# Performance work log

Measured on AMD Instinct MI355X. Metric: run time of the kernel, lower is better.

## Reference

```python
import jax, jax.numpy as jnp
import numpy as np

D, K, B, IMG, NCH = 128, 512, 8, 128, 3


def adder2d(x, w, k, stride, pad):
    # AdderNet L1 'convolution': y[b,co,l] = -sum_p |patch[b,p,l] - w[co,p]|
    # x: [B,C,H,W], w: [Cout, C*k*k]
    p = jax.lax.conv_general_dilated_patches(x, (k, k), (stride, stride), [(pad, pad), (pad, pad)])
    Bb, P, Ho, Wo = p.shape
    p = p.reshape(Bb, P, Ho * Wo)  # [B, C*k*k, L]
    def one(wc):  # wc: [P] -> [B, L]; sequential over Cout to bound memory
        return -jnp.sum(jnp.abs(p - wc[None, :, None]), axis=1)
    o = jax.lax.map(one, w)  # [Cout, B, L]
    return jnp.transpose(o, (1, 0, 2)).reshape(Bb, w.shape[0], Ho, Wo)


def bn(x, g, b, eps=1e-5):
    # eval-mode BatchNorm2d with running_mean=0, running_var=1
    s = g * jax.lax.rsqrt(jnp.asarray(1.0 + eps, x.dtype))
    return x * s[None, :, None, None] + b[None, :, None, None]


def conv2d(x, w, b, pad):
    y = jax.lax.conv_general_dilated(x, w, (1, 1), [(pad, pad), (pad, pad)],
                                     dimension_numbers=('NCHW', 'OIHW', 'NCHW'))
    return y + b[None, :, None, None]


def up2x(x):  # nn.Upsample(scale_factor=2, bilinear, align_corners=False)
    Bb, C, H, W = x.shape
    return jax.image.resize(x, (Bb, C, 2 * H, 2 * W), method='bilinear')


def adder_resblock(x, w1, w2, g, b):
    # [ReLU, adder3x3, BN, ReLU, adder1x1] + residual
    h = jax.nn.relu(x)
    h = adder2d(h, w1, 3, 1, 1)
    h = bn(h, g, b)
    h = jax.nn.relu(h)
    h = adder2d(h, w2, 1, 1, 0)
    return x + h


def conv_resblock(x, w1, b1, w2, b2):
    # [ReLU, conv3x3, ReLU, conv1x1] + residual (bn=False in decoder)
    h = jax.nn.relu(x)
    h = conv2d(h, w1, b1, 1)
    h = jax.nn.relu(h)
    h = conv2d(h, w2, b2, 0)
    return x + h


def vq_forward(z_e, E):
    # NearestEmbed: E is [d, k]
    Bb, C, H, W = z_e.shape
    flat = jnp.transpose(z_e, (0, 2, 3, 1)).reshape(-1, C)  # [N, d]
    d2 = (jnp.sum(flat * flat, axis=1, keepdims=True)
          - 2.0 * (flat @ E) + jnp.sum(E * E, axis=0)[None, :])  # [N, k]
    argmin = jnp.argmin(d2, axis=1)  # [N]
    q = jnp.take(E.T, argmin, axis=0)  # [N, d]
    # weight_sg=True path: straight-through to z_e, no grad to E
    zq_flat = flat + jax.lax.stop_gradient(q - flat)
    z_q = jnp.transpose(zq_flat.reshape(Bb, H, W, C), (0, 3, 1, 2))
    # emb path: z_e detached, grad flows to E through the gather
    emb = jnp.transpose(q.reshape(Bb, H, W, C), (0, 3, 1, 2))
    return z_q, emb, argmin.reshape(Bb, H, W)


def reference(x, we1, we2, ae1_w1, ae1_w2, ae2_w1, ae2_w2, bn_gamma, bn_beta,
              emb_weight, rd1_w1, rd1_b1, rd1_w2, rd1_b2, rd2_w1, rd2_b1,
              rd2_w2, rd2_b2, cd1_w, cd1_b, cd2_w, cd2_b):
    g, b = bn_gamma, bn_beta
    h = adder2d(x, we1, 4, 2, 1)
    h = jax.nn.relu(bn(h, g[0], b[0]))
    h = adder2d(h, we2, 4, 2, 1)
    h = jax.nn.relu(bn(h, g[1], b[1]))
    h = adder_resblock(h, ae1_w1, ae1_w2, g[2], b[2])
    h = bn(h, g[3], b[3])
    h = adder_resblock(h, ae2_w1, ae2_w2, g[4], b[4])
    z_e = bn(h, g[5], b[5])  # bne4 (gamma = 1/40)

    z_q, emb, argmin = vq_forward(z_e, emb_weight)

    y = conv_resblock(z_q, rd1_w1, rd1_b1, rd1_w2, rd1_b2)
    y = bn(y, g[6], b[6])
    y = conv_resblock(y, rd2_w1, rd2_b1, rd2_w2, rd2_b2)
    y = up2x(y)
    y = conv2d(y, cd1_w, cd1_b, 1)
    y = jax.nn.relu(bn(y, g[7], b[7]))
    y = up2x(y)
    y = conv2d(y, cd2_w, cd2_b, 1)
    y = jnp.tanh(y)
    return (y, z_e, emb, argmin)


def setup_inputs() -> dict:
    key = jax.random.key(0)
    ks = jax.random.split(key, 16)
    f = lambda k, shp: (0.02 * jax.random.normal(k, shp)).astype(jnp.float32)
    inp = {}
    inp['x'] = jax.random.normal(ks[0], (B, NCH, IMG, IMG), jnp.float32)
    inp['we1'] = f(ks[1], (D, NCH * 16))       # adder 4x4 s2
    inp['we2'] = f(ks[2], (D, D * 16))
    inp['ae1_w1'] = f(ks[3], (D, D * 9))       # adder 3x3
    inp['ae1_w2'] = f(ks[4], (D, D))           # adder 1x1
    inp['ae2_w1'] = f(ks[5], (D, D * 9))
    inp['ae2_w2'] = f(ks[6], (D, D))
    inp['bn_gamma'] = jnp.ones((8, D), jnp.float32).at[5].set(1.0 / 40.0)
    inp['bn_beta'] = jnp.zeros((8, D), jnp.float32)
    inp['emb_weight'] = f(ks[7], (D, K))
    inp['rd1_w1'] = f(ks[8], (D, D, 3, 3)); inp['rd1_b1'] = jnp.zeros(D, jnp.float32)
    inp['rd1_w2'] = f(ks[9], (D, D, 1, 1)); inp['rd1_b2'] = jnp.zeros(D, jnp.float32)
    inp['rd2_w1'] = f(ks[10], (D, D, 3, 3)); inp['rd2_b1'] = jnp.zeros(D, jnp.float32)
    inp['rd2_w2'] = f(ks[11], (D, D, 1, 1)); inp['rd2_b2'] = jnp.zeros(D, jnp.float32)
    inp['cd1_w'] = f(ks[12], (D, D, 3, 3)); inp['cd1_b'] = jnp.zeros(D, jnp.float32)
    inp['cd2_w'] = f(ks[13], (NCH, D, 3, 3)); inp['cd2_b'] = jnp.zeros(NCH, jnp.float32)
    return inp
```

## Files before the change

### kernel.cpp

```cpp
#include <hip/hip_runtime.h>
#include <math.h>

constexpr int Dc = 128;
constexpr int Kc = 512;
constexpr int Bc = 8;

template<int ISADD, int K, int STRIDE, int PAD, int IT, int EPI, int CIN, int CH,
         int OUT_ROWS, int WOUT, int WIN, int HIN, int HOUT, int COBW, int NW,
         int KSPLIT>
__global__ __launch_bounds__(NW * 64)
void lds_layer(const float* __restrict__ x, const float* __restrict__ w,
               const float* __restrict__ bias,
               const float* __restrict__ itG, const float* __restrict__ itB,
               const float* __restrict__ res,
               const float* __restrict__ rG, const float* __restrict__ rB,
               const float* __restrict__ oG, const float* __restrict__ oB,
               float* __restrict__ out) {
  constexpr int BT = NW * 64;
  constexpr int NWG = NW / KSPLIT;
  constexpr int CINW = CIN / KSPLIT;
  constexpr int CHS = KSPLIT * CH;
  constexpr int PW = 2;
  constexpr int KK = K * K;
  constexpr int SPAN = (PW - 1) * STRIDE + K;
  constexpr int IN_ROWS = (OUT_ROWS - 1) * STRIDE + K;
  constexpr int WPAD = (WOUT - 1) * STRIDE + K;
  constexpr int WLDS = (WPAD + 3) & ~3;
  constexpr int PGW = WOUT / PW;
  static_assert(OUT_ROWS * PGW == 64, "one wave covers the pixel tile");
  static_assert(NW % KSPLIT == 0 && CIN % KSPLIT == 0 && CINW % CH == 0, "split");
  static_assert(KSPLIT == 1 ||
                NWG * 64 * PW * COBW <= CHS * IN_ROWS * WLDS, "scratch fits");
  constexpr int NBAND = HOUT / OUT_ROWS;
  constexpr int W4 = WIN / 4;
  constexpr int NELEM4 = CHS * IN_ROWS * W4;
  constexpr int NIT4 = (NELEM4 + BT - 1) / BT;
  constexpr bool EXACT = (NELEM4 % BT) == 0;
  const float r15 = rsqrtf(1.0f + 1e-5f);

  __shared__ alignas(16) float lds[CHS][IN_ROWS][WLDS];

  int tid = threadIdx.x;
  int gb = blockIdx.x;
  int cg = gb / (Bc * NBAND);
  int rem = gb % (Bc * NBAND);
  int band = rem % NBAND;
  int b = rem / NBAND;
  int wv = __builtin_amdgcn_readfirstlane(tid >> 6);
  int lane = tid & 63;
  int grp = wv / NWG;
  int wloc = wv % NWG;
  int co0 = cg * (NWG * COBW) + wloc * COBW;
  int pr = lane / PGW, pc = lane % PGW;
  int oh = band * OUT_ROWS + pr;
  int ow0 = pc * PW;
  int yi0 = band * OUT_ROWS * STRIDE - PAD;

  for (int e = tid; e < CHS * IN_ROWS * WLDS; e += BT) ((float*)lds)[e] = 0.f;

  float acc[PW][COBW];
#pragma unroll
  for (int p = 0; p < PW; ++p)
#pragma unroll
    for (int j = 0; j < COBW; ++j)
      acc[p][j] = (ISADD || grp != 0) ? 0.f : bias[co0 + j];

  const float* xb = x + (long)b * CIN * HIN * WIN;
  float4 rbuf[NIT4];

  auto stage = [&](int cc) {
#pragma unroll
    for (int it = 0; it < NIT4; ++it) {
      int e = it * BT + tid;
      if (!EXACT && e >= NELEM4) break;
      int c4 = e % W4;
      int r = (e / W4) % IN_ROWS;
      int ch2 = e / (W4 * IN_ROWS);
      int gc = cc + (ch2 % CH) + (ch2 / CH) * CINW;
      int yi = yi0 + r;
      float4 v = make_float4(0.f, 0.f, 0.f, 0.f);
      if (yi >= 0 && yi < HIN) {
        v = *(const float4*)&xb[((long)gc * HIN + yi) * WIN + 4 * c4];
        if (IT == 1) {
          v.x = fmaxf(v.x, 0.f); v.y = fmaxf(v.y, 0.f);
          v.z = fmaxf(v.z, 0.f); v.w = fmaxf(v.w, 0.f);
        }
        if (IT == 2) {
          float sc = itG[gc] * r15, bc = itB[gc];
          v.x = fmaxf(fmaf(v.x, sc, bc), 0.f);
          v.y = fmaxf(fmaf(v.y, sc, bc), 0.f);
          v.z = fmaxf(fmaf(v.z, sc, bc), 0.f);
          v.w = fmaxf(fmaf(v.w, sc, bc), 0.f);
        }
      }
      rbuf[it] = v;
    }
  };
  auto towrite = [&]() {
#pragma unroll
    for (int it = 0; it < NIT4; ++it) {
      int e = it * BT + tid;
      if (!EXACT && e >= NELEM4) break;
      int c4 = e % W4;
      int r = (e / W4) % IN_ROWS;
      int ch2 = e / (W4 * IN_ROWS);
      float* p = &lds[ch2][r][4 * c4 + PAD];
      float4 v = rbuf[it];
      p[0] = v.x; p[1] = v.y; p[2] = v.z; p[3] = v.w;
    }
  };

  stage(0);
  for (int cc = 0; cc < CINW; cc += CH) {
    __syncthreads();
    towrite();
    __syncthreads();
    if (cc + CH < CINW) stage(cc + CH);
    for (int chl = 0; chl < CH; ++chl) {
      float vbuf[K][SPAN];
#pragma unroll
      for (int kh = 0; kh < K; ++kh) {
        const float* rp0 = &lds[grp * CH + chl][pr * STRIDE + kh][ow0 * STRIDE];
        if constexpr (SPAN == 6 && (PW * STRIDE) % 4 == 0) {
          float4 a = *(const float4*)rp0;
          float2 c2 = *(const float2*)(rp0 + 4);
          vbuf[kh][0] = a.x; vbuf[kh][1] = a.y; vbuf[kh][2] = a.z;
          vbuf[kh][3] = a.w; vbuf[kh][4] = c2.x; vbuf[kh][5] = c2.y;
        } else if constexpr (SPAN == 4 && (PW * STRIDE) % 2 == 0) {
          float2 a = *(const float2*)rp0;
          float2 c2 = *(const float2*)(rp0 + 2);
          vbuf[kh][0] = a.x; vbuf[kh][1] = a.y;
          vbuf[kh][2] = c2.x; vbuf[kh][3] = c2.y;
        } else if constexpr (SPAN == 2 && (PW * STRIDE) % 2 == 0) {
          float2 a = *(const float2*)rp0;
          vbuf[kh][0] = a.x; vbuf[kh][1] = a.y;
        } else {
#pragma unroll
          for (int s = 0; s < SPAN; ++s) vbuf[kh][s] = rp0[s];
        }
      }
      const float* wc = w + ((long)co0 * CIN + (grp * CINW + cc + chl)) * KK;
#pragma unroll
      for (int kh = 0; kh < K; ++kh)
#pragma unroll
        for (int kw = 0; kw < K; ++kw)
#pragma unroll
          for (int j = 0; j < COBW; ++j) {
            float ww = wc[(long)j * CIN * KK + kh * K + kw];
#pragma unroll
            for (int p = 0; p < PW; ++p) {
              float v = vbuf[kh][p * STRIDE + kw];
              if (ISADD) acc[p][j] += fabsf(v - ww);
              else       acc[p][j] = fmaf(v, ww, acc[p][j]);
            }
          }
    }
  }

  if constexpr (KSPLIT >= 2) {
    float* scr = (float*)lds;
    int sb = (wloc * 64 + lane) * (PW * COBW);
#pragma unroll
    for (int g = 1; g < KSPLIT; ++g) {
      __syncthreads();
      if (grp == g) {
#pragma unroll
        for (int p = 0; p < PW; ++p)
#pragma unroll
          for (int j = 0; j < COBW; ++j) scr[sb + p * COBW + j] = acc[p][j];
      }
      __syncthreads();
      if (grp == 0) {
#pragma unroll
        for (int p = 0; p < PW; ++p)
#pragma unroll
          for (int j = 0; j < COBW; ++j) acc[p][j] += scr[sb + p * COBW + j];
      }
    }
    if (grp != 0) return;
  }

  long obase = ((long)(b * Dc + co0) * HOUT + oh) * WOUT + ow0;
  float* ob = out + obase;
  const float* rp = (EPI == 2 || EPI == 3 || EPI == 6) ? res + obase : nullptr;
  constexpr long hw = (long)HOUT * WOUT;
#pragma unroll
  for (int j = 0; j < COBW; ++j) {
    float og = 0.f, obb = 0.f, rg = 0.f, rbb = 0.f;
    if (EPI == 1 || EPI == 6) { og = oG[co0 + j] * r15; obb = oB[co0 + j]; }
    if (EPI == 3 || EPI == 6) { rg = rG[co0 + j] * r15; rbb = rB[co0 + j]; }
#pragma unroll
    for (int p = 0; p < PW; ++p) {
      float val = ISADD ? -acc[p][j] : acc[p][j];
      if (EPI == 1) val = fmaxf(fmaf(val, og, obb), 0.f);
      if (EPI == 2) val = rp[j * hw + p] + val;
      if (EPI == 3) val = fmaf(rp[j * hw + p], rg, rbb) + val;
      if (EPI == 5) val = fmaxf(val, 0.f);
      if (EPI == 6) val = fmaf(fmaf(rp[j * hw + p], rg, rbb) + val, og, obb);
      ob[j * hw + p] = val;
    }
  }
}

__device__ __forceinline__ void up_coef(int p, int H, int& i0, int& i1, float& w0, float& w1) {
  int m = p >> 1;
  if ((p & 1) == 0) { i0 = (m > 0) ? m - 1 : 0; i1 = m; w0 = 0.25f; w1 = 0.75f; }
  else              { i0 = m; i1 = (m + 1 < H) ? m + 1 : H - 1; w0 = 0.75f; w1 = 0.25f; }
}

__global__ void up2x_kernel(const float* __restrict__ in, float* __restrict__ out,
                            int C, int H, int W) {
  int H2 = 2 * H, W2 = 2 * W;
  int i = blockIdx.x * blockDim.x + threadIdx.x;
  int total = Bc * C * H2 * W2;
  if (i >= total) return;
  int ow = i % W2; int t = i / W2;
  int oh = t % H2; t /= H2;
  int c = t % C; int b = t / C;
  int y0, y1, x0, x1; float wy0, wy1, wx0, wx1;
  up_coef(oh, H, y0, y1, wy0, wy1);
  up_coef(ow, W, x0, x1, wx0, wx1);
  const float* p = in + (b * C + c) * H * W;
  float v = wy0 * (wx0 * p[y0 * W + x0] + wx1 * p[y0 * W + x1])
          + wy1 * (wx0 * p[y1 * W + x0] + wx1 * p[y1 * W + x1]);
  out[i] = v;
}

__global__ __launch_bounds__(256)
void conv3x3_up_tanh_quad(const float* __restrict__ x, const float* __restrict__ w,
                          const float* __restrict__ bias, float* __restrict__ out,
                          int Hs, int Ws, int Cout) {
  constexpr int CIN = Dc;
  int H2 = 2 * Hs, W2 = 2 * Ws;
  int nq = Hs * Ws;
  int i = blockIdx.x * blockDim.x + threadIdx.x;
  int total = Bc * Cout * nq;
  if (i >= total) return;
  int q = i % nq; int t = i / nq;
  int co = t % Cout; int b = t / Cout;
  int n = q % Ws, m = q / Ws;
  int rows[3] = { (m > 0) ? m - 1 : 0, m, (m + 1 < Hs) ? m + 1 : Hs - 1 };
  int cols[3] = { (n > 0) ? n - 1 : 0, n, (n + 1 < Ws) ? n + 1 : Ws - 1 };
  float rv[4] = { (2 * m - 1 >= 0) ? 1.f : 0.f, 1.f, 1.f, (2 * m + 2 < H2) ? 1.f : 0.f };
  float cv[4] = { (2 * n - 1 >= 0) ? 1.f : 0.f, 1.f, 1.f, (2 * n + 2 < W2) ? 1.f : 0.f };
  float bco = bias[co];
  float acc[4] = { bco, bco, bco, bco };
  const float* xb = x + b * CIN * nq;
  const float* wb = w + co * CIN * 9;
  for (int c = 0; c < CIN; ++c) {
    const float* xc = xb + c * nq;
    float s[3][3];
#pragma unroll
    for (int a = 0; a < 3; ++a)
#pragma unroll
      for (int e = 0; e < 3; ++e) s[a][e] = xc[rows[a] * Ws + cols[e]];
    float rb[4][3];
#pragma unroll
    for (int e = 0; e < 3; ++e) {
      rb[0][e] = fmaf(0.75f, s[0][e], 0.25f * s[1][e]);
      rb[1][e] = fmaf(0.25f, s[0][e], 0.75f * s[1][e]);
      rb[2][e] = fmaf(0.75f, s[1][e], 0.25f * s[2][e]);
      rb[3][e] = fmaf(0.25f, s[1][e], 0.75f * s[2][e]);
    }
    float u[4][4];
#pragma unroll
    for (int di = 0; di < 4; ++di) {
      float rm = rv[di];
      u[di][0] = fmaf(0.75f, rb[di][0], 0.25f * rb[di][1]) * rm * cv[0];
      u[di][1] = fmaf(0.25f, rb[di][0], 0.75f * rb[di][1]) * rm * cv[1];
      u[di][2] = fmaf(0.75f, rb[di][1], 0.25f * rb[di][2]) * rm * cv[2];
      u[di][3] = fmaf(0.25f, rb[di][1], 0.75f * rb[di][2]) * rm * cv[3];
    }
    const float* wc = wb + c * 9;
#pragma unroll
    for (int kh = 0; kh < 3; ++kh)
#pragma unroll
      for (int kw = 0; kw < 3; ++kw) {
        float ww = wc[kh * 3 + kw];
        acc[0] = fmaf(u[kh][kw],         ww, acc[0]);
        acc[1] = fmaf(u[kh][kw + 1],     ww, acc[1]);
        acc[2] = fmaf(u[kh + 1][kw],     ww, acc[2]);
        acc[3] = fmaf(u[kh + 1][kw + 1], ww, acc[3]);
      }
  }
  float* ob = out + (b * Cout + co) * H2 * W2 + (2 * m) * W2 + 2 * n;
  ob[0] = tanhf(acc[0]);      ob[1] = tanhf(acc[1]);
  ob[W2] = tanhf(acc[2]);     ob[W2 + 1] = tanhf(acc[3]);
}

__global__ void vq_e2_kernel(const float* __restrict__ E, float* __restrict__ e2) {
  int k = blockIdx.x * blockDim.x + threadIdx.x;
  if (k >= Kc) return;
  float s = 0.f;
  for (int d = 0; d < Dc; ++d) { float v = E[d * Kc + k]; s += v * v; }
  e2[k] = s;
}

__global__ __launch_bounds__(256)
void vq_kernel8(const float* __restrict__ z_e, const float* __restrict__ E,
                const float* __restrict__ e2,
                float* __restrict__ emb, float* __restrict__ argmin_out) {
  constexpr int HW = 1024;
  __shared__ float f[8][Dc];
  __shared__ float d2s[8][256];
  __shared__ int   ks[8][256];
  int tid = threadIdx.x;
  int n0 = blockIdx.x * 8;
  int b = n0 >> 10;
  int rem = n0 & 1023;
  const float* zb = z_e + (long)b * Dc * HW + rem;
#pragma unroll
  for (int i = 0; i < 4; ++i) {
    int e = i * 256 + tid;
    int p = e & 7, d = e >> 3;
    f[p][d] = zb[d * HW + p];
  }
  __syncthreads();
  float f2 = 0.f;
  if (tid < 8) {
    for (int d = 0; d < Dc; ++d) f2 += f[tid][d] * f[tid][d];
    d2s[tid][0] = f2;
  }
  __syncthreads();
  float f2v[8];
#pragma unroll
  for (int p = 0; p < 8; ++p) f2v[p] = d2s[p][0];
  __syncthreads();

  float best[8]; int bk[8];
#pragma unroll
  for (int p = 0; p < 8; ++p) { best[p] = 3.4e38f; bk[p] = 0; }
  for (int kk = tid; kk < Kc; kk += 256) {
    float dot[8];
#pragma unroll
    for (int p = 0; p < 8; ++p) dot[p] = 0.f;
    for (int d = 0; d < Dc; ++d) {
      float ed = E[d * Kc + kk];
#pragma unroll
      for (int p = 0; p < 8; ++p) dot[p] = fmaf(f[p][d], ed, dot[p]);
    }
    float e2k = e2[kk];
#pragma unroll
    for (int p = 0; p < 8; ++p) {
      float d2 = f2v[p] - 2.f * dot[p] + e2k;
      if (d2 < best[p] || (d2 == best[p] && kk < bk[p])) { best[p] = d2; bk[p] = kk; }
    }
  }
#pragma unroll
  for (int p = 0; p < 8; ++p) { d2s[p][tid] = best[p]; ks[p][tid] = bk[p]; }
  __syncthreads();
  for (int s = 128; s > 0; s >>= 1) {
    if (tid < s) {
#pragma unroll
      for (int p = 0; p < 8; ++p) {
        float ob = d2s[p][tid + s]; int ok = ks[p][tid + s];
        if (ob < d2s[p][tid] || (ob == d2s[p][tid] && ok < ks[p][tid])) {
          d2s[p][tid] = ob; ks[p][tid] = ok;
        }
      }
    }
    __syncthreads();
  }
  if (tid < 8) argmin_out[n0 + tid] = (float)ks[tid][0];
  float* eb = emb + (long)b * Dc * HW + rem;
#pragma unroll
  for (int i = 0; i < 4; ++i) {
    int e = i * 256 + tid;
    int p = e & 7, d = e >> 3;
    eb[d * HW + p] = E[d * Kc + ks[p][0]];
  }
}

extern "C" void kernel_launch(void* const* d_in, const int* in_sizes, int n_in,
                              void* d_out, int out_size, void* d_ws, size_t ws_size,
                              hipStream_t stream) {
  const float* x      = (const float*)d_in[0];
  const float* we1    = (const float*)d_in[1];
  const float* we2    = (const float*)d_in[2];
  const float* ae1_w1 = (const float*)d_in[3];
  const float* ae1_w2 = (const float*)d_in[4];
  const float* ae2_w1 = (const float*)d_in[5];
  const float* ae2_w2 = (const float*)d_in[6];
  const float* bn_g   = (const float*)d_in[7];
  const float* bn_b   = (const float*)d_in[8];
  const float* embw   = (const float*)d_in[9];
  const float* rd1_w1 = (const float*)d_in[10];
  const float* rd1_b1 = (const float*)d_in[11];
  const float* rd1_w2 = (const float*)d_in[12];
  const float* rd1_b2 = (const float*)d_in[13];
  const float* rd2_w1 = (const float*)d_in[14];
  const float* rd2_b1 = (const float*)d_in[15];
  const float* rd2_w2 = (const float*)d_in[16];
  const float* rd2_b2 = (const float*)d_in[17];
  const float* cd1_w  = (const float*)d_in[18];
  const float* cd1_b  = (const float*)d_in[19];
  const float* cd2_w  = (const float*)d_in[20];
  const float* cd2_b  = (const float*)d_in[21];

  const float* g0 = bn_g + 0 * Dc; const float* b0 = bn_b + 0 * Dc;
  const float* g1 = bn_g + 1 * Dc; const float* b1 = bn_b + 1 * Dc;
  const float* g2 = bn_g + 2 * Dc; const float* b2 = bn_b + 2 * Dc;
  const float* g3 = bn_g + 3 * Dc; const float* b3 = bn_b + 3 * Dc;
  const float* g4 = bn_g + 4 * Dc; const float* b4 = bn_b + 4 * Dc;
  const float* g5 = bn_g + 5 * Dc; const float* b5 = bn_b + 5 * Dc;
  const float* g6 = bn_g + 6 * Dc; const float* b6 = bn_b + 6 * Dc;
  const float* g7 = bn_g + 7 * Dc; const float* b7 = bn_b + 7 * Dc;

  float* W64a = (float*)d_ws;
  float* W64b = W64a + 4194304;
  float* Wa   = W64b + 4194304;
  float* Wb   = Wa + 1048576;
  float* Wc   = Wb + 1048576;
  float* e2b  = W64b;

  float* out_y   = (float*)d_out;
  float* out_ze  = out_y  + 393216;
  float* out_emb = out_ze + 1048576;
  float* out_am  = out_emb + 1048576;

  const int TB = 256;
  const int TB8 = 512;
  auto nb = [](int n) { return (n + 255) / 256; };
  const int N64 = Bc * Dc * 64 * 64;
  const float* nul = nullptr;

  const int G32s = 16 * Bc * 8;
  const int G11s = 8 * Bc * 8;
  const int Gwe1 = 8 * Bc * 32;
  const int Gcd1 = 4 * Bc * 32;

  lds_layer<1,4,2,1, 0,1, 3,3, 2,64,128,128,64, 4,4,1><<<Gwe1, TB, 0, stream>>>(
      x, we1, nul, nul, nul, nul, nul, nul, g0, b0, W64a);
  lds_layer<1,4,2,1, 0,1, Dc,2, 4,32,64,64,32, 4,8,4><<<G32s, TB8, 0, stream>>>(
      W64a, we2, nul, nul, nul, nul, nul, nul, g1, b1, Wa);
  lds_layer<1,3,1,1, 0,1, Dc,8, 4,32,32,32,32, 4,8,4><<<G32s, TB8, 0, stream>>>(
      Wa, ae1_w1, nul, nul, nul, nul, nul, nul, g2, b2, Wb);
  lds_layer<1,1,1,0, 0,2, Dc,16, 4,32,32,32,32, 8,8,4><<<G11s, TB8, 0, stream>>>(
      Wb, ae1_w2, nul, nul, nul, Wa, nul, nul, nul, nul, Wc);
  lds_layer<1,3,1,1, 2,1, Dc,8, 4,32,32,32,32, 4,8,4><<<G32s, TB8, 0, stream>>>(
      Wc, ae2_w1, nul, g3, b3, nul, nul, nul, g4, b4, Wb);
  lds_layer<1,1,1,0, 0,6, Dc,16, 4,32,32,32,32, 8,8,4><<<G11s, TB8, 0, stream>>>(
      Wb, ae2_w2, nul, nul, nul, Wc, g3, b3, g5, b5, out_ze);

  vq_e2_kernel<<<2, 256, 0, stream>>>(embw, e2b);
  vq_kernel8<<<Bc * 1024 / 8, 256, 0, stream>>>(out_ze, embw, e2b, out_emb, out_am);

  lds_layer<0,3,1,1, 1,5, Dc,8, 4,32,32,32,32, 4,8,4><<<G32s, TB8, 0, stream>>>(
      out_emb, rd1_w1, rd1_b1, nul, nul, nul, nul, nul, nul, nul, Wb);
  lds_layer<0,1,1,0, 0,2, Dc,16, 4,32,32,32,32, 8,8,4><<<G11s, TB8, 0, stream>>>(
      Wb, rd1_w2, rd1_b2, nul, nul, out_emb, nul, nul, nul, nul, Wa);
  lds_layer<0,3,1,1, 2,5, Dc,8, 4,32,32,32,32, 4,8,4><<<G32s, TB8, 0, stream>>>(
      Wa, rd2_w1, rd2_b1, g6, b6, nul, nul, nul, nul, nul, Wb);
  lds_layer<0,1,1,0, 0,3, Dc,16, 4,32,32,32,32, 8,8,4><<<G11s, TB8, 0, stream>>>(
      Wb, rd2_w2, rd2_b2, nul, nul, Wa, g6, b6, nul, nul, Wc);

  up2x_kernel<<<nb(N64), TB, 0, stream>>>(Wc, W64a, Dc, 32, 32);
  lds_layer<0,3,1,1, 0,1, Dc,8, 2,64,64,64,64, 8,8,2><<<Gcd1, TB8, 0, stream>>>(
      W64a, cd1_w, cd1_b, nul, nul, nul, nul, nul, g7, b7, W64b);

  conv3x3_up_tanh_quad<<<nb(Bc * 3 * 64 * 64), TB, 0, stream>>>(W64b, cd2_w, cd2_b, out_y, 64, 64, 3);
}
```

Measured before the change: 852.3 us.

## Add dedicated 1x1 pointwise kernel and retune LDS layer split factors

Adds a pw1x1 kernel for the four 1x1 adder/conv layers. It reads input pixels directly from global memory as float2, splits the channel reduction across 4 waves, and combines partial sums through shared memory before applying the fused epilogue. The 3x3 and 4x4 lds_layer launches are retuned to larger channel chunks, fewer output channels per workgroup and a smaller K-split. The goal is to cut LDS staging overhead for pointwise layers and improve occupancy and parallelism for the spatial layers, at the cost of weights being read from global or cache per thread.

```diff
diff --git a/kernel.cpp b/kernel.cpp
--- a/kernel.cpp
+++ b/kernel.cpp
@@ -202,6 +202,91 @@
   }
 }
 
+template<int ISADD, int EPI, int COBW>
+__global__ __launch_bounds__(256)
+void pw1x1(const float* __restrict__ x, const float* __restrict__ w,
+           const float* __restrict__ bias,
+           const float* __restrict__ res,
+           const float* __restrict__ rG, const float* __restrict__ rB,
+           const float* __restrict__ oG, const float* __restrict__ oB,
+           float* __restrict__ out) {
+  constexpr int HW = 1024;
+  constexpr int CIN = Dc;
+  constexpr int KS = 4;
+  constexpr int CSEG = CIN / KS;
+  constexpr int PXB = 128;
+  constexpr int NPG = HW / PXB;
+  constexpr int OPT = (PXB * COBW) / 256;
+  static_assert(OPT * 256 == PXB * COBW, "combine exact");
+  const float r15 = rsqrtf(1.0f + 1e-5f);
+
+  __shared__ float scr[KS][COBW][PXB];
+
+  int tid = threadIdx.x;
+  int wv = __builtin_amdgcn_readfirstlane(tid >> 6);
+  int lane = tid & 63;
+  int gb = blockIdx.x;
+  int cg = gb / (Bc * NPG);
+  int rem = gb % (Bc * NPG);
+  int pg = rem % NPG;
+  int b = rem / NPG;
+  int co0 = cg * COBW;
+  int px = pg * PXB + lane * 2;
+
+  const float* xc = x + ((long)b * CIN + wv * CSEG) * HW + px;
+  const float* wseg = w + wv * CSEG;
+
+  float acc[2][COBW];
+#pragma unroll
+  for (int p = 0; p < 2; ++p)
+#pragma unroll
+    for (int j = 0; j < COBW; ++j) acc[p][j] = 0.f;
+
+#pragma unroll 4
+  for (int c = 0; c < CSEG; ++c) {
+    float2 v = *(const float2*)&xc[(long)c * HW];
+#pragma unroll
+    for (int j = 0; j < COBW; ++j) {
+      float ww = wseg[(long)(co0 + j) * CIN + c];
+      if (ISADD) {
+        acc[0][j] += fabsf(v.x - ww);
+        acc[1][j] += fabsf(v.y - ww);
+      } else {
+        acc[0][j] = fmaf(v.x, ww, acc[0][j]);
+        acc[1][j] = fmaf(v.y, ww, acc[1][j]);
+      }
+    }
+  }
+
+#pragma unroll
+  for (int j = 0; j < COBW; ++j) {
+    float2 t = make_float2(acc[0][j], acc[1][j]);
+    *(float2*)&scr[wv][j][lane * 2] = t;
+  }
+  __syncthreads();
+
+#pragma unroll
+  for (int k = 0; k < OPT; ++k) {
+    int e = k * 256 + tid;
+    int pxl = e % PXB;
+    int j = e / PXB;
+    float s = scr[0][j][pxl] + scr[1][j][pxl] + scr[2][j][pxl] + scr[3][j][pxl];
+    float val = ISADD ? -s : s + bias[co0 + j];
+    long oidx = ((long)b * Dc + co0 + j) * HW + pg * PXB + pxl;
+    if (EPI == 2) val = res[oidx] + val;
+    if (EPI == 3) {
+      float rg = rG[co0 + j] * r15, rbb = rB[co0 + j];
+      val = fmaf(res[oidx], rg, rbb) + val;
+    }
+    if (EPI == 6) {
+      float rg = rG[co0 + j] * r15, rbb = rB[co0 + j];
+      float og = oG[co0 + j] * r15, obb = oB[co0 + j];
+      val = fmaf(fmaf(res[oidx], rg, rbb) + val, og, obb);
+    }
+    out[oidx] = val;
+  }
+}
+
 __device__ __forceinline__ void up_coef(int p, int H, int& i0, int& i1, float& w0, float& w1) {
   int m = p >> 1;
   if ((p & 1) == 0) { i0 = (m > 0) ? m - 1 : 0; i1 = m; w0 = 0.25f; w1 = 0.75f; }
@@ -425,34 +510,34 @@
   const float* nul = nullptr;
 
   const int G32s = 16 * Bc * 8;
-  const int G11s = 8 * Bc * 8;
   const int Gwe1 = 8 * Bc * 32;
   const int Gcd1 = 4 * Bc * 32;
+  const int Gpw  = 32 * Bc * 8;
 
   lds_layer<1,4,2,1, 0,1, 3,3, 2,64,128,128,64, 4,4,1><<<Gwe1, TB, 0, stream>>>(
       x, we1, nul, nul, nul, nul, nul, nul, g0, b0, W64a);
-  lds_layer<1,4,2,1, 0,1, Dc,2, 4,32,64,64,32, 4,8,4><<<G32s, TB8, 0, stream>>>(
+  lds_layer<1,4,2,1, 0,1, Dc,4, 4,32,64,64,32, 2,8,2><<<G32s, TB8, 0, stream>>>(
       W64a, we2, nul, nul, nul, nul, nul, nul, g1, b1, Wa);
-  lds_layer<1,3,1,1, 0,1, Dc,8, 4,32,32,32,32, 4,8,4><<<G32s, TB8, 0, stream>>>(
+  lds_layer<1,3,1,1, 0,1, Dc,16, 4,32,32,32,32, 2,8,2><<<G32s, TB8, 0, stream>>>(
       Wa, ae1_w1, nul, nul, nul, nul, nul, nul, g2, b2, Wb);
-  lds_layer<1,1,1,0, 0,2, Dc,16, 4,32,32,32,32, 8,8,4><<<G11s, TB8, 0, stream>>>(
-      Wb, ae1_w2, nul, nul, nul, Wa, nul, nul, nul, nul, Wc);
-  lds_layer<1,3,1,1, 2,1, Dc,8, 4,32,32,32,32, 4,8,4><<<G32s, TB8, 0, stream>>>(
+  pw1x1<1,2,4><<<Gpw, TB, 0, stream>>>(
+      Wb, ae1_w2, nul, Wa, nul, nul, nul, nul, Wc);
+  lds_layer<1,3,1,1, 2,1, Dc,16, 4,32,32,32,32, 2,8,2><<<G32s, TB8, 0, stream>>>(
       Wc, ae2_w1, nul, g3, b3, nul, nul, nul, g4, b4, Wb);
-  lds_layer<1,1,1,0, 0,6, Dc,16, 4,32,32,32,32, 8,8,4><<<G11s, TB8, 0, stream>>>(
-      Wb, ae2_w2, nul, nul, nul, Wc, g3, b3, g5, b5, out_ze);
+  pw1x1<1,6,4><<<Gpw, TB, 0, stream>>>(
+      Wb, ae2_w2, nul, Wc, g3, b3, g5, b5, out_ze);
 
   vq_e2_kernel<<<2, 256, 0, stream>>>(embw, e2b);
   vq_kernel8<<<Bc * 1024 / 8, 256, 0, stream>>>(out_ze, embw, e2b, out_emb, out_am);
 
-  lds_layer<0,3,1,1, 1,5, Dc,8, 4,32,32,32,32, 4,8,4><<<G32s, TB8, 0, stream>>>(
+  lds_layer<0,3,1,1, 1,5, Dc,16, 4,32,32,32,32, 2,8,2><<<G32s, TB8, 0, stream>>>(
       out_emb, rd1_w1, rd1_b1, nul, nul, nul, nul, nul, nul, nul, Wb);
-  lds_layer<0,1,1,0, 0,2, Dc,16, 4,32,32,32,32, 8,8,4><<<G11s, TB8, 0, stream>>>(
-      Wb, rd1_w2, rd1_b2, nul, nul, out_emb, nul, nul, nul, nul, Wa);
-  lds_layer<0,3,1,1, 2,5, Dc,8, 4,32,32,32,32, 4,8,4><<<G32s, TB8, 0, stream>>>(
+  pw1x1<0,2,4><<<Gpw, TB, 0, stream>>>(
+      Wb, rd1_w2, rd1_b2, out_emb, nul, nul, nul, nul, Wa);
+  lds_layer<0,3,1,1, 2,5, Dc,16, 4,32,32,32,32, 2,8,2><<<G32s, TB8, 0, stream>>>(
       Wa, rd2_w1, rd2_b1, g6, b6, nul, nul, nul, nul, nul, Wb);
-  lds_layer<0,1,1,0, 0,3, Dc,16, 4,32,32,32,32, 8,8,4><<<G11s, TB8, 0, stream>>>(
-      Wb, rd2_w2, rd2_b2, nul, nul, Wa, g6, b6, nul, nul, Wc);
+  pw1x1<0,3,4><<<Gpw, TB, 0, stream>>>(
+      Wb, rd2_w2, rd2_b2, Wa, g6, b6, nul, nul, Wc);
 
   up2x_kernel<<<nb(N64), TB, 0, stream>>>(Wc, W64a, Dc, 32, 32);
   lds_layer<0,3,1,1, 0,1, Dc,8, 2,64,64,64,64, 8,8,2><<<Gcd1, TB8, 0, stream>>>(
```

After: 830.9 us. 1.03x faster.
